# Performance work log

Measured on AMD Instinct MI355X. Metric: run time of the kernel, lower is better.

The kernel has to match this reference:

```python
import jax, jax.numpy as jnp
import numpy as np

NUM_USERS = 100000
NUM_ITEMS = 50000
NUM_HIDDEN = 64
NUM_BINS = 10
BATCH = 131072
N_QUAD = 64  # quadrature nodes in incomplete/complete beta
EPS = 1e-6


def _trapz0(y, dt):
    # trapezoidal rule along axis 0 with uniform spacing dt
    return (jnp.sum(y, axis=0) - 0.5 * (y[0] + y[-1])) * dt


def setup_inputs() -> dict:
    key = jax.random.key(0)
    ks = jax.random.split(key, 12)
    return {
        "uid_input": jax.random.randint(ks[0], (BATCH,), 0, NUM_USERS),
        "iid_input": jax.random.randint(ks[1], (BATCH,), 0, NUM_ITEMS),
        "uid_features": 0.1 * jax.random.normal(ks[2], (NUM_USERS, NUM_HIDDEN + 1), jnp.float32),
        "iid_features": 0.1 * jax.random.normal(ks[3], (NUM_ITEMS, NUM_HIDDEN + 1), jnp.float32),
        "uid_bin_terms": 0.1 * jax.random.normal(ks[4], (NUM_USERS, NUM_BINS), jnp.float32),
        "iid_bin_terms": 0.1 * jax.random.normal(ks[5], (NUM_ITEMS, NUM_BINS), jnp.float32),
        "uid_alpha_emb": 0.01 * jax.random.normal(ks[6], (NUM_USERS, 1), jnp.float32),
        "uid_beta_emb": 0.01 * jax.random.normal(ks[7], (NUM_USERS, 1), jnp.float32),
        "iid_alpha_emb": 0.01 * jax.random.normal(ks[8], (NUM_ITEMS, 1), jnp.float32),
        "iid_beta_emb": 0.01 * jax.random.normal(ks[9], (NUM_ITEMS, 1), jnp.float32),
        "global_bias": jnp.asarray(2.0, jnp.float32),
    }


def reference(uid_input, iid_input, uid_features, iid_features,
              uid_bin_terms, iid_bin_terms, uid_alpha_emb, uid_beta_emb,
              iid_alpha_emb, iid_beta_emb, global_bias):
    # embedding lookups (confidence features alias the regular features)
    uf = uid_features[uid_input]          # (B, H+1)
    vf = iid_features[iid_input]          # (B, H+1)
    u = uf[:, :-1]                        # (B, H)
    v = vf[:, :-1]

    # mu / upsilon (upsilon_layer_id == 2: |dot|)
    dot = jnp.sum(u * v, axis=-1, keepdims=True)                    # (B, 1)
    len_prod = (jnp.linalg.norm(u, axis=1, keepdims=True)
                * jnp.linalg.norm(v, axis=1, keepdims=True))
    mu = jnp.clip(0.5 + 0.5 * dot / jnp.maximum(len_prod, EPS), EPS, 1.0 - EPS)
    upsilon = jnp.maximum(jnp.abs(dot), EPS)

    # alpha / beta
    alpha = jnp.maximum(0.01, mu * upsilon)
    beta = jnp.maximum(0.01, upsilon - alpha)
    alpha = global_bias + alpha
    beta = global_bias + beta
    alpha = jnp.maximum(0.01, alpha + uid_alpha_emb[uid_input] + iid_alpha_emb[iid_input])  # (B,1)
    beta = jnp.maximum(0.01, beta + uid_beta_emb[uid_input] + iid_beta_emb[iid_input])      # (B,1)

    # per-pair bin edges via normalized exp + cumsum
    terms = jnp.exp(uid_bin_terms[uid_input] + iid_bin_terms[iid_input])  # (B, NUM_BINS)
    terms = terms / jnp.sum(terms, axis=-1, keepdims=True)
    edges = jnp.cumsum(terms, axis=-1)                                    # (B, NUM_BINS)

    # regularized incomplete beta at interior edges via trapezoidal quadrature
    x = edges[:, :-1]                                  # (B, NB-1)
    t = jnp.linspace(0.0, 1.0, N_QUAD, dtype=alpha.dtype)
    dt = t[1] - t[0]
    t3 = t[:, None, None]                              # (n, 1, 1)
    a3 = alpha[None, :, :]                             # (1, B, 1)
    b3 = beta[None, :, :]
    tx = t3 * x[None]                                  # (n, B, NB-1)
    integrand = (tx ** (a3 - 1.0)) * ((1.0 - tx) ** (b3 - 1.0))
    integrand = integrand * (t3 <= x[None]).astype(integrand.dtype)
    Bx_ab = _trapz0(integrand, dt)                     # (B, NB-1)

    # complete beta B(a, b)
    c_int = (t[None, :] ** (alpha - 1.0)) * ((1.0 - t[None, :]) ** (beta - 1.0))  # (B, n)
    B_ab = (jnp.sum(c_int, axis=-1) - 0.5 * (c_int[:, 0] + c_int[:, -1])) * dt    # (B,)

    cdf = Bx_ab / B_ab[:, None]                        # (B, NB-1)
    cdf = jnp.concatenate([cdf, jnp.ones_like(alpha)], axis=-1)  # (B, NB)
    mass = jnp.concatenate([cdf[:, :1], cdf[:, 1:] - cdf[:, :-1]], axis=-1)
    return mass
```

## Files before the change

### kernel.cpp

```cpp
#include <hip/hip_runtime.h>
#include <math.h>

#define BLOCK 256

struct F4a4 { float a, b, c, d; };

__device__ __forceinline__ float exp2_fast(float x) {
#if __has_builtin(__builtin_amdgcn_exp2f)
    return __builtin_amdgcn_exp2f(x);
#else
    return __expf(x * 0.69314718055994531f);
#endif
}

__global__ __launch_bounds__(BLOCK) void lbd_kernel(
    const int* __restrict__ uid_in, const int* __restrict__ iid_in,
    const float* __restrict__ uf,  const float* __restrict__ vf,
    const float* __restrict__ ubt, const float* __restrict__ ibt,
    const float* __restrict__ uae, const float* __restrict__ ube,
    const float* __restrict__ iae, const float* __restrict__ ibe,
    const float* __restrict__ gbp, float* __restrict__ out, int B)
{
    __shared__ float2 s_tl[64];
    __shared__ float2 s_ll[64];
    __shared__ float  s_out[BLOCK * 10];

    const int tid = threadIdx.x;
    if (tid < 64) {
        const double step = 1.0 / 63.0;
        float tf = (float)((double)tid * step);
        if (tid == 63) tf = 1.0f;
        float lt = __log2f(tf);
        float l1 = __log2f(1.0f - tf);
        s_tl[tid] = make_float2(tf, lt);
        s_ll[tid] = make_float2(lt, l1);
    }
    __syncthreads();

    const int gid = blockIdx.x * BLOCK + tid;
    float mass[10];
#pragma unroll
    for (int j = 0; j < 10; ++j) mass[j] = 0.0f;

    if (gid < B) {
        const int u = uid_in[gid];
        const int v = iid_in[gid];

        const float* pu = uf + (long long)u * 65;
        const float* pv = vf + (long long)v * 65;
        float dot = 0.f, su = 0.f, sv = 0.f;
#pragma unroll
        for (int k = 0; k < 16; ++k) {
            F4a4 a = ((const F4a4*)pu)[k];
            F4a4 b = ((const F4a4*)pv)[k];
            dot += a.a * b.a + a.b * b.b + a.c * b.c + a.d * b.d;
            su  += a.a * a.a + a.b * a.b + a.c * a.c + a.d * a.d;
            sv  += b.a * b.a + b.b * b.b + b.c * b.c + b.d * b.d;
        }

        const float gb = gbp[0];
        const float len_prod = sqrtf(su) * sqrtf(sv);
        const float EPS = 1e-6f;
        const float HI  = (float)(1.0 - 1e-6);
        float mu = 0.5f + (0.5f * dot) / fmaxf(len_prod, EPS);
        mu = fminf(fmaxf(mu, EPS), HI);
        const float ups = fmaxf(fabsf(dot), EPS);
        const float al0 = fmaxf(0.01f, mu * ups);
        const float be0 = fmaxf(0.01f, ups - al0);
        const float alpha = fmaxf(0.01f, (gb + al0) + uae[u] + iae[v]);
        const float beta  = fmaxf(0.01f, (gb + be0) + ube[u] + ibe[v]);
        const float am1 = alpha - 1.0f;
        const float bm1 = beta  - 1.0f;

        const float* pb = ubt + (long long)u * 10;
        const float* qb = ibt + (long long)v * 10;
        double tmd[10];
#pragma unroll
        for (int k = 0; k < 10; ++k)
            tmd[k] = exp((double)pb[k] + (double)qb[k]);
        double ssum = 0.0;
#pragma unroll
        for (int k = 0; k < 10; ++k) ssum = ssum + tmd[k];
        double xs[9];
        {
            double c = 0.0;
#pragma unroll
            for (int j = 0; j < 9; ++j) {
                c = c + tmd[j] / ssum;
                xs[j] = c;
            }
        }

        float d0 = 0.f, d1 = 0.f, d2 = 0.f, d3 = 0.f;
        {
            int i = 1;
            for (; i + 3 <= 62; i += 4) {
                float2 l0 = s_ll[i], l1v = s_ll[i + 1], l2 = s_ll[i + 2], l3 = s_ll[i + 3];
                d0 += exp2_fast(fmaf(am1, l0.x,  bm1 * l0.y));
                d1 += exp2_fast(fmaf(am1, l1v.x, bm1 * l1v.y));
                d2 += exp2_fast(fmaf(am1, l2.x,  bm1 * l2.y));
                d3 += exp2_fast(fmaf(am1, l3.x,  bm1 * l3.y));
            }
            for (; i <= 62; ++i) {
                float2 l0 = s_ll[i];
                d0 += exp2_fast(fmaf(am1, l0.x, bm1 * l0.y));
            }
        }
        const float dtf = (float)(1.0 / 63.0);
        const float Bab = ((d0 + d1) + (d2 + d3)) * dtf;

        const double STEP = 1.0 / 63.0;
        float cdf[9];
#pragma unroll
        for (int j = 0; j < 9; ++j) {
            const double x  = xs[j];
            const float  xf = (float)x;
            const float  lx = __log2f(xf);
            const float  alx = am1 * lx;
            int im = (int)(x * 63.0);
            if (im > 62) im = 62;
            while (im < 62 && (double)(im + 1) * STEP <= x) ++im;
            while (im >= 1 && (double)im * STEP > x) --im;
            float a0 = 0.f, a1 = 0.f, a2 = 0.f, a3 = 0.f;
            int i = 1;
            for (; i + 3 <= im; i += 4) {
                float2 t0 = s_tl[i], t1 = s_tl[i + 1], t2 = s_tl[i + 2], t3 = s_tl[i + 3];
                a0 += exp2_fast(fmaf(bm1, __log2f(fmaf(-t0.x, xf, 1.0f)), fmaf(am1, t0.y, alx)));
                a1 += exp2_fast(fmaf(bm1, __log2f(fmaf(-t1.x, xf, 1.0f)), fmaf(am1, t1.y, alx)));
                a2 += exp2_fast(fmaf(bm1, __log2f(fmaf(-t2.x, xf, 1.0f)), fmaf(am1, t2.y, alx)));
                a3 += exp2_fast(fmaf(bm1, __log2f(fmaf(-t3.x, xf, 1.0f)), fmaf(am1, t3.y, alx)));
            }
            for (; i <= im; ++i) {
                float2 t0 = s_tl[i];
                a0 += exp2_fast(fmaf(bm1, __log2f(fmaf(-t0.x, xf, 1.0f)), fmaf(am1, t0.y, alx)));
            }
            const float s = (a0 + a1) + (a2 + a3);
            cdf[j] = (s * dtf) / Bab;
        }

        mass[0] = cdf[0];
#pragma unroll
        for (int j = 1; j < 9; ++j) mass[j] = cdf[j] - cdf[j - 1];
        mass[9] = 1.0f - cdf[8];
    }

#pragma unroll
    for (int j = 0; j < 10; ++j) s_out[tid * 10 + j] = mass[j];
    __syncthreads();
    const long long base = (long long)blockIdx.x * (BLOCK * 10);
#pragma unroll
    for (int r = 0; r < 10; ++r) {
        const int idx = r * BLOCK + tid;
        const long long g = base + idx;
        if (g < (long long)B * 10) out[g] = s_out[idx];
    }
}

extern "C" void kernel_launch(void* const* d_in, const int* in_sizes, int n_in,
                              void* d_out, int out_size, void* d_ws, size_t ws_size,
                              hipStream_t stream) {
    (void)n_in; (void)out_size; (void)d_ws; (void)ws_size;
    const int*   uid = (const int*)d_in[0];
    const int*   iid = (const int*)d_in[1];
    const float* uf  = (const float*)d_in[2];
    const float* vf  = (const float*)d_in[3];
    const float* ubt = (const float*)d_in[4];
    const float* ibt = (const float*)d_in[5];
    const float* uae = (const float*)d_in[6];
    const float* ube = (const float*)d_in[7];
    const float* iae = (const float*)d_in[8];
    const float* ibe = (const float*)d_in[9];
    const float* gb  = (const float*)d_in[10];
    float* out = (float*)d_out;
    const int B = in_sizes[0];
    const int grid = (B + BLOCK - 1) / BLOCK;
    hipLaunchKernelGGL(lbd_kernel, dim3(grid), dim3(BLOCK), 0, stream,
                       uid, iid, uf, vf, ubt, ibt, uae, ube, iae, ibe, gb, out, B);
}
```

Measured before the change: 148.4 us.

## Split each sample across 16 lanes with masked fixed-length quadrature

Each sample is now handled by 16 threads instead of one. The feature gathers, dot-product and norm reductions, softmax prefix scan and quadrature nodes are distributed across lanes and combined with wave shuffles. The variable-length per-edge quadrature loops become a fixed 64-node sweep with predication, which removes lane divergence and the shared-memory tables and output staging. The cost is evaluating all nodes for every edge, roughly twice the useful transcendental work. The complete-beta sum also now includes the endpoint nodes, and these only contribute zero when alpha-1 and beta-1 are positive.

Result: faster. 136.1 us (-8.3%).

```diff
diff --git a/kernel.cpp b/kernel.cpp
--- a/kernel.cpp
+++ b/kernel.cpp
@@ -2,8 +2,6 @@
 #include <math.h>
 
 #define BLOCK 256
-
-struct F4a4 { float a, b, c, d; };
 
 __device__ __forceinline__ float exp2_fast(float x) {
 #if __has_builtin(__builtin_amdgcn_exp2f)
@@ -21,139 +19,126 @@
     const float* __restrict__ iae, const float* __restrict__ ibe,
     const float* __restrict__ gbp, float* __restrict__ out, int B)
 {
-    __shared__ float2 s_tl[64];
-    __shared__ float2 s_ll[64];
-    __shared__ float  s_out[BLOCK * 10];
+    const int tid = threadIdx.x;
+    const int sub = tid & 15;
+    const int s   = blockIdx.x * (BLOCK / 16) + (tid >> 4);
+    if (s >= B) return;
 
-    const int tid = threadIdx.x;
-    if (tid < 64) {
-        const double step = 1.0 / 63.0;
-        float tf = (float)((double)tid * step);
-        if (tid == 63) tf = 1.0f;
-        float lt = __log2f(tf);
-        float l1 = __log2f(1.0f - tf);
-        s_tl[tid] = make_float2(tf, lt);
-        s_ll[tid] = make_float2(lt, l1);
+    const int u = uid_in[s];
+    const int v = iid_in[s];
+
+    const long long ub = (long long)u * 65;
+    const long long vb = (long long)v * 65;
+    float fu0 = uf[ub + sub],      fv0 = vf[vb + sub];
+    float fu1 = uf[ub + 16 + sub], fv1 = vf[vb + 16 + sub];
+    float fu2 = uf[ub + 32 + sub], fv2 = vf[vb + 32 + sub];
+    float fu3 = uf[ub + 48 + sub], fv3 = vf[vb + 48 + sub];
+
+    float dotp = fu0 * fv0 + fu1 * fv1 + fu2 * fv2 + fu3 * fv3;
+    float sup  = fu0 * fu0 + fu1 * fu1 + fu2 * fu2 + fu3 * fu3;
+    float svp  = fv0 * fv0 + fv1 * fv1 + fv2 * fv2 + fv3 * fv3;
+#pragma unroll
+    for (int d = 1; d < 16; d <<= 1) {
+        dotp += __shfl_xor(dotp, d, 64);
+        sup  += __shfl_xor(sup,  d, 64);
+        svp  += __shfl_xor(svp,  d, 64);
     }
-    __syncthreads();
 
-    const int gid = blockIdx.x * BLOCK + tid;
-    float mass[10];
+    const float gb = gbp[0];
+    const float len_prod = sqrtf(sup) * sqrtf(svp);
+    const float EPS = 1e-6f;
+    const float HI  = (float)(1.0 - 1e-6);
+    float mu = 0.5f + (0.5f * dotp) / fmaxf(len_prod, EPS);
+    mu = fminf(fmaxf(mu, EPS), HI);
+    const float ups = fmaxf(fabsf(dotp), EPS);
+    const float al0 = fmaxf(0.01f, mu * ups);
+    const float be0 = fmaxf(0.01f, ups - al0);
+    const float alpha = fmaxf(0.01f, (gb + al0) + uae[u] + iae[v]);
+    const float beta  = fmaxf(0.01f, (gb + be0) + ube[u] + ibe[v]);
+    const float am1 = alpha - 1.0f;
+    const float bm1 = beta  - 1.0f;
+
+    const double STEP = 1.0 / 63.0;
+    float xf_own = 0.f, lx_own = 0.f;
+    int   im_own = 0;
+    {
+        double e = 0.0;
+        if (sub < 10)
+            e = exp((double)ubt[u * 10 + sub] + (double)ibt[v * 10 + sub]);
+        double c = e;
 #pragma unroll
-    for (int j = 0; j < 10; ++j) mass[j] = 0.0f;
-
-    if (gid < B) {
-        const int u = uid_in[gid];
-        const int v = iid_in[gid];
-
-        const float* pu = uf + (long long)u * 65;
-        const float* pv = vf + (long long)v * 65;
-        float dot = 0.f, su = 0.f, sv = 0.f;
-#pragma unroll
-        for (int k = 0; k < 16; ++k) {
-            F4a4 a = ((const F4a4*)pu)[k];
-            F4a4 b = ((const F4a4*)pv)[k];
-            dot += a.a * b.a + a.b * b.b + a.c * b.c + a.d * b.d;
-            su  += a.a * a.a + a.b * a.b + a.c * a.c + a.d * a.d;
-            sv  += b.a * b.a + b.b * b.b + b.c * b.c + b.d * b.d;
+        for (int d = 1; d < 16; d <<= 1) {
+            double t = __shfl_up(c, d, 16);
+            if (sub >= d) c += t;
         }
-
-        const float gb = gbp[0];
-        const float len_prod = sqrtf(su) * sqrtf(sv);
-        const float EPS = 1e-6f;
-        const float HI  = (float)(1.0 - 1e-6);
-        float mu = 0.5f + (0.5f * dot) / fmaxf(len_prod, EPS);
-        mu = fminf(fmaxf(mu, EPS), HI);
-        const float ups = fmaxf(fabsf(dot), EPS);
-        const float al0 = fmaxf(0.01f, mu * ups);
-        const float be0 = fmaxf(0.01f, ups - al0);
-        const float alpha = fmaxf(0.01f, (gb + al0) + uae[u] + iae[v]);
-        const float beta  = fmaxf(0.01f, (gb + be0) + ube[u] + ibe[v]);
-        const float am1 = alpha - 1.0f;
-        const float bm1 = beta  - 1.0f;
-
-        const float* pb = ubt + (long long)u * 10;
-        const float* qb = ibt + (long long)v * 10;
-        double tmd[10];
-#pragma unroll
-        for (int k = 0; k < 10; ++k)
-            tmd[k] = exp((double)pb[k] + (double)qb[k]);
-        double ssum = 0.0;
-#pragma unroll
-        for (int k = 0; k < 10; ++k) ssum = ssum + tmd[k];
-        double xs[9];
-        {
-            double c = 0.0;
-#pragma unroll
-            for (int j = 0; j < 9; ++j) {
-                c = c + tmd[j] / ssum;
-                xs[j] = c;
-            }
-        }
-
-        float d0 = 0.f, d1 = 0.f, d2 = 0.f, d3 = 0.f;
-        {
-            int i = 1;
-            for (; i + 3 <= 62; i += 4) {
-                float2 l0 = s_ll[i], l1v = s_ll[i + 1], l2 = s_ll[i + 2], l3 = s_ll[i + 3];
-                d0 += exp2_fast(fmaf(am1, l0.x,  bm1 * l0.y));
-                d1 += exp2_fast(fmaf(am1, l1v.x, bm1 * l1v.y));
-                d2 += exp2_fast(fmaf(am1, l2.x,  bm1 * l2.y));
-                d3 += exp2_fast(fmaf(am1, l3.x,  bm1 * l3.y));
-            }
-            for (; i <= 62; ++i) {
-                float2 l0 = s_ll[i];
-                d0 += exp2_fast(fmaf(am1, l0.x, bm1 * l0.y));
-            }
-        }
-        const float dtf = (float)(1.0 / 63.0);
-        const float Bab = ((d0 + d1) + (d2 + d3)) * dtf;
-
-        const double STEP = 1.0 / 63.0;
-        float cdf[9];
-#pragma unroll
-        for (int j = 0; j < 9; ++j) {
-            const double x  = xs[j];
-            const float  xf = (float)x;
-            const float  lx = __log2f(xf);
-            const float  alx = am1 * lx;
+        const double ssum = __shfl(c, 9, 16);
+        if (sub < 9) {
+            const double x = c / ssum;
             int im = (int)(x * 63.0);
             if (im > 62) im = 62;
             while (im < 62 && (double)(im + 1) * STEP <= x) ++im;
             while (im >= 1 && (double)im * STEP > x) --im;
-            float a0 = 0.f, a1 = 0.f, a2 = 0.f, a3 = 0.f;
-            int i = 1;
-            for (; i + 3 <= im; i += 4) {
-                float2 t0 = s_tl[i], t1 = s_tl[i + 1], t2 = s_tl[i + 2], t3 = s_tl[i + 3];
-                a0 += exp2_fast(fmaf(bm1, __log2f(fmaf(-t0.x, xf, 1.0f)), fmaf(am1, t0.y, alx)));
-                a1 += exp2_fast(fmaf(bm1, __log2f(fmaf(-t1.x, xf, 1.0f)), fmaf(am1, t1.y, alx)));
-                a2 += exp2_fast(fmaf(bm1, __log2f(fmaf(-t2.x, xf, 1.0f)), fmaf(am1, t2.y, alx)));
-                a3 += exp2_fast(fmaf(bm1, __log2f(fmaf(-t3.x, xf, 1.0f)), fmaf(am1, t3.y, alx)));
-            }
-            for (; i <= im; ++i) {
-                float2 t0 = s_tl[i];
-                a0 += exp2_fast(fmaf(bm1, __log2f(fmaf(-t0.x, xf, 1.0f)), fmaf(am1, t0.y, alx)));
-            }
-            const float s = (a0 + a1) + (a2 + a3);
-            cdf[j] = (s * dtf) / Bab;
+            im_own = im;
+            xf_own = (float)x;
+            lx_own = __log2f(xf_own);
         }
+    }
+    float xfj[9], alxj[9];
+    int   imj[9];
+#pragma unroll
+    for (int j = 0; j < 9; ++j) {
+        xfj[j]  = __shfl(xf_own, j, 16);
+        alxj[j] = am1 * __shfl(lx_own, j, 16);
+        imj[j]  = __shfl(im_own, j, 16);
+    }
 
-        mass[0] = cdf[0];
+    float tfm[4], ltm[4], l1m[4];
 #pragma unroll
-        for (int j = 1; j < 9; ++j) mass[j] = cdf[j] - cdf[j - 1];
-        mass[9] = 1.0f - cdf[8];
+    for (int m = 0; m < 4; ++m) {
+        const int i = m * 16 + sub;
+        const float tf = (float)((double)i * STEP);
+        tfm[m] = tf;
+        ltm[m] = __log2f(tf);
+        l1m[m] = __log2f(1.0f - tf);
+    }
+
+    float acc[10];
+#pragma unroll
+    for (int j = 0; j < 10; ++j) acc[j] = 0.0f;
+
+#pragma unroll
+    for (int m = 0; m < 4; ++m) {
+        const int   i    = m * 16 + sub;
+        const float t    = tfm[m];
+        const float altm = am1 * ltm[m];
+        acc[9] += exp2_fast(fmaf(am1, ltm[m], bm1 * l1m[m]));
+#pragma unroll
+        for (int j = 0; j < 9; ++j) {
+            const float e = fmaf(bm1, __log2f(fmaf(-t, xfj[j], 1.0f)), altm + alxj[j]);
+            const float y = exp2_fast(e);
+            const bool ok = (unsigned)(i - 1) < (unsigned)imj[j];
+            acc[j] += ok ? y : 0.0f;
+        }
     }
 
 #pragma unroll
-    for (int j = 0; j < 10; ++j) s_out[tid * 10 + j] = mass[j];
-    __syncthreads();
-    const long long base = (long long)blockIdx.x * (BLOCK * 10);
+    for (int d = 1; d < 16; d <<= 1) {
 #pragma unroll
-    for (int r = 0; r < 10; ++r) {
-        const int idx = r * BLOCK + tid;
-        const long long g = base + idx;
-        if (g < (long long)B * 10) out[g] = s_out[idx];
+        for (int j = 0; j < 10; ++j) acc[j] += __shfl_xor(acc[j], d, 64);
     }
+
+    const float dtf = (float)(1.0 / 63.0);
+    const float Bab = acc[9] * dtf;
+    const float rB  = 1.0f / Bab;
+    float cdfv[9];
+#pragma unroll
+    for (int j = 0; j < 9; ++j) cdfv[j] = (acc[j] * dtf) * rB;
+
+    float mo = cdfv[0];
+#pragma unroll
+    for (int j = 1; j < 9; ++j) mo = (sub == j) ? (cdfv[j] - cdfv[j - 1]) : mo;
+    mo = (sub == 9) ? (1.0f - cdfv[8]) : mo;
+    if (sub < 10) out[(long long)s * 10 + sub] = mo;
 }
 
 extern "C" void kernel_launch(void* const* d_in, const int* in_sizes, int n_in,
@@ -173,7 +158,8 @@
     const float* gb  = (const float*)d_in[10];
     float* out = (float*)d_out;
     const int B = in_sizes[0];
-    const int grid = (B + BLOCK - 1) / BLOCK;
+    const int samples_per_block = BLOCK / 16;
+    const int grid = (B + samples_per_block - 1) / samples_per_block;
     hipLaunchKernelGGL(lbd_kernel, dim3(grid), dim3(BLOCK), 0, stream,
                        uid, iid, uf, vf, ubt, ibt, uae, ube, iae, ibe, gb, out, B);
 }
```
